# Kernel optimization log

Measured on AMD Instinct MI355X. Metric: run time of the kernel, lower is better.

## Reference

```python
import jax, jax.numpy as jnp
import numpy as np

N = 100000   # graph nodes
E = 600000   # edges
D = 128      # feature_dim
K = 3        # candidate ops per MixedOp
EPS = 1e-5   # BatchNorm eps


def _param_stack(key, n_ops):
    kW, kb = jax.random.split(key)
    W = jax.random.normal(kW, (n_ops, K, D, D), jnp.float32) * (1.0 / np.sqrt(D))
    b = jax.random.normal(kb, (n_ops, K, D), jnp.float32) * 0.01
    g = jnp.ones((n_ops, K, D), jnp.float32)
    be = jnp.zeros((n_ops, K, D), jnp.float32)
    return W, b, g, be


def setup_inputs() -> dict:
    key = jax.random.key(0)
    ks = jax.random.split(key, 16)
    inp = {
        'src_emb': jax.random.normal(ks[0], (N, D), jnp.float32),
        'hr': jax.random.normal(ks[1], (N, D), jnp.float32),
        'edge_src': jax.random.randint(ks[2], (E,), 0, N),
        'edge_dst': jax.random.randint(ks[3], (E,), 0, N),
        'weights_zero': jax.random.uniform(ks[4], (1, K), jnp.float32),
        'weights_first': jax.random.uniform(ks[5], (3, K), jnp.float32),
        'weights_middle': jax.random.uniform(ks[6], (2, K), jnp.float32),
        'weights_last': jax.random.uniform(ks[7], (2, K), jnp.float32),
    }
    for name, k, n_ops in [('zero', ks[8], 1), ('first', ks[9], 3), ('mid', ks[10], 2), ('last', ks[11], 2)]:
        W, b, g, be = _param_stack(k, n_ops)
        inp[f'W_{name}'] = W; inp[f'b_{name}'] = b
        inp[f'g_{name}'] = g; inp[f'be_{name}'] = be
    inp['W_cat'] = jax.random.normal(ks[12], (3 * D, D), jnp.float32) * (1.0 / np.sqrt(3 * D))
    inp['b_cat'] = jax.random.normal(ks[13], (D,), jnp.float32) * 0.01
    inp['g_cat'] = jnp.ones((D,), jnp.float32)
    inp['be_cat'] = jnp.zeros((D,), jnp.float32)
    return inp


def _mean_agg(h, src, dst):
    s = jax.ops.segment_sum(h[src], dst, num_segments=N)            # [N,D]
    deg = jax.ops.segment_sum(jnp.ones((src.shape[0],), h.dtype), dst, num_segments=N)
    return s / jnp.maximum(deg, 1.0)[:, None]


def _max_agg(h, src, dst):
    m = jax.ops.segment_max(h[src], dst, num_segments=N)            # -inf for empty segs
    return jnp.where(jnp.isfinite(m), m, 0.0)


def _mixed(cands, w, W, b, g, be):
    # cands: list of K [N,D]; w:[K]; W:[K,D,D]; b/g/be:[K,D]
    x = jnp.stack(cands)                                            # [K,N,D]
    y = jnp.einsum('knd,kdf->knf', x, W) + b[:, None, :]            # Linear per candidate
    mu = jnp.mean(y, axis=1, keepdims=True)                         # BatchNorm1d (batch stats)
    var = jnp.var(y, axis=1, keepdims=True)
    y = (y - mu) * jax.lax.rsqrt(var + EPS) * g[:, None, :] + be[:, None, :]
    y = jax.nn.relu(y)
    return jnp.einsum('k,knd->nd', w, y)                            # alpha-weighted sum


def _graph_cands(h, src, dst):
    return [h, _mean_agg(h, src, dst), _max_agg(h, src, dst)]


def _cell_forward(src_emb, hr, edge_src, edge_dst,
                  weights_zero, weights_first, weights_middle, weights_last,
                  W_zero, b_zero, g_zero, be_zero,
                  W_first, b_first, g_first, be_first,
                  W_mid, b_mid, g_mid, be_mid,
                  W_last, b_last, g_last, be_last,
                  W_cat, b_cat, g_cat, be_cat):
    src, dst = edge_src, edge_dst
    # Cell_Zero: relation-composition candidates on (src_emb, hr)
    pre = [src_emb, src_emb - hr, src_emb * hr]
    h_in = _mixed(pre, weights_zero[0], W_zero[0], b_zero[0], g_zero[0], be_zero[0])
    # Cell_First (nodes=2): ops layout [(i=0,j=0),(i=1,j=0),(i=1,j=1)]
    states = [h_in]
    s0 = _mixed(_graph_cands(states[0], src, dst), weights_first[0], W_first[0], b_first[0], g_first[0], be_first[0])
    states.append(s0)
    s1 = (_mixed(_graph_cands(states[0], src, dst), weights_first[1], W_first[1], b_first[1], g_first[1], be_first[1])
          + _mixed(_graph_cands(states[1], src, dst), weights_first[2], W_first[2], b_first[2], g_first[2], be_first[2]))
    states.append(s1)
    states = states[1:]                                             # drop h_in -> len 2
    # Cell_Middle (nodes=2): one MixedOp per state
    states = [_mixed(_graph_cands(states[i], src, dst), weights_middle[i], W_mid[i], b_mid[i], g_mid[i], be_mid[i])
              for i in range(2)]
    # Cell_Last (in_nodes=2, nodes=1): one new state from both inputs; returns all 3
    s_last = (_mixed(_graph_cands(states[0], src, dst), weights_last[0], W_last[0], b_last[0], g_last[0], be_last[0])
              + _mixed(_graph_cands(states[1], src, dst), weights_last[1], W_last[1], b_last[1], g_last[1], be_last[1]))
    states = states + [s_last]                                      # len 3
    # concat -> Linear -> BN -> ReLU (dropout p=0)
    h = jnp.concatenate(states, axis=1) @ W_cat + b_cat             # [N,D]
    mu = jnp.mean(h, axis=0, keepdims=True)
    var = jnp.var(h, axis=0, keepdims=True)
    h = (h - mu) * jax.lax.rsqrt(var + EPS) * g_cat + be_cat
    return jax.nn.relu(h)


def reference(src_emb, hr, edge_src, edge_dst,
              weights_zero, weights_first, weights_middle, weights_last,
              W_zero, b_zero, g_zero, be_zero,
              W_first, b_first, g_first, be_first,
              W_mid, b_mid, g_mid, be_mid,
              W_last, b_last, g_last, be_last,
              W_cat, b_cat, g_cat, be_cat):
    return _cell_forward(src_emb, hr, edge_src, edge_dst,
                         weights_zero, weights_first, weights_middle, weights_last,
                         W_zero, b_zero, g_zero, be_zero,
                         W_first, b_first, g_first, be_first,
                         W_mid, b_mid, g_mid, be_mid,
                         W_last, b_last, g_last, be_last,
                         W_cat, b_cat, g_cat, be_cat)
```

## Files before the change

### kernel.cpp

```cpp
#include <hip/hip_runtime.h>

#define N_NODES 100000
#define N_EDGES 600000
#define NPAD    100096
#define NTILES  782
#define SCAN_B  98
#define EPS_F   1e-5f

typedef __bf16 bf16_t;
typedef __bf16 bf16x8 __attribute__((ext_vector_type(8)));
typedef __bf16 bf16x4 __attribute__((ext_vector_type(4)));
typedef float  f32x4  __attribute__((ext_vector_type(4)));

__global__ __launch_bounds__(256)
void init_zero_kernel(int* __restrict__ deg, float* __restrict__ stats)
{
    int i = blockIdx.x * 256 + threadIdx.x;
    if (i < N_NODES) deg[i] = 0;
    if (i < 9 * 768) stats[i] = 0.f;
}

__global__ __launch_bounds__(256)
void transpose_w_kernel(const float* __restrict__ Wz, const float* __restrict__ Wf,
                        const float* __restrict__ Wm, const float* __restrict__ Wl,
                        const float* __restrict__ Wc, bf16_t* __restrict__ wt)
{
    int idx = blockIdx.x * 256 + threadIdx.x;
    int mat = idx >> 14;
    int off = idx & 16383;
    int n = off >> 7, kk = off & 127;
    const float* src;
    if      (mat < 3)  src = Wz + mat * 16384;
    else if (mat < 12) src = Wf + (mat - 3) * 16384;
    else if (mat < 18) src = Wm + (mat - 12) * 16384;
    else if (mat < 24) src = Wl + (mat - 18) * 16384;
    else               src = Wc + (mat - 24) * 16384;
    wt[idx] = (bf16_t)src[kk * 128 + n];
}

__global__ __launch_bounds__(256)
void pre_kernel(const float* __restrict__ se, const float* __restrict__ hr,
                bf16_t* __restrict__ p0, bf16_t* __restrict__ p1, bf16_t* __restrict__ p2)
{
    long i = ((long)blockIdx.x * 256 + threadIdx.x) * 8;
    float4 a0 = *(const float4*)&se[i], a1 = *(const float4*)&se[i + 4];
    float4 b0 = *(const float4*)&hr[i], b1 = *(const float4*)&hr[i + 4];
    float av[8] = {a0.x, a0.y, a0.z, a0.w, a1.x, a1.y, a1.z, a1.w};
    float bv[8] = {b0.x, b0.y, b0.z, b0.w, b1.x, b1.y, b1.z, b1.w};
    bf16x8 o0, o1, o2;
#pragma unroll
    for (int j = 0; j < 8; ++j) {
        o0[j] = (bf16_t)av[j];
        o1[j] = (bf16_t)(av[j] - bv[j]);
        o2[j] = (bf16_t)(av[j] * bv[j]);
    }
    *(bf16x8*)&p0[i] = o0;
    *(bf16x8*)&p1[i] = o1;
    *(bf16x8*)&p2[i] = o2;
}

__global__ __launch_bounds__(256)
void deg_count_kernel(const int* __restrict__ dst, int* __restrict__ deg)
{
    int i = blockIdx.x * 256 + threadIdx.x;
    if (i < N_EDGES) atomicAdd(&deg[dst[i]], 1);
}

__global__ __launch_bounds__(256)
void scan_a_kernel(const int* __restrict__ deg, int* __restrict__ partials)
{
    __shared__ int ls[256];
    int b = blockIdx.x, t = threadIdx.x;
    int s = 0;
    for (int j = 0; j < 4; ++j) {
        int i = b * 1024 + t * 4 + j;
        if (i < N_NODES) s += deg[i];
    }
    ls[t] = s; __syncthreads();
    for (int o = 128; o > 0; o >>= 1) {
        if (t < o) ls[t] += ls[t + o];
        __syncthreads();
    }
    if (t == 0) partials[b] = ls[0];
}

__global__ void scan_b_kernel(const int* __restrict__ partials, int* __restrict__ pofs)
{
    if (threadIdx.x == 0) {
        int a = 0;
        for (int i = 0; i < SCAN_B; ++i) { pofs[i] = a; a += partials[i]; }
    }
}

__global__ __launch_bounds__(256)
void scan_c_kernel(const int* __restrict__ deg, const int* __restrict__ pofs,
                   int* __restrict__ row_ptr, int* __restrict__ cursor)
{
    __shared__ int ls[256];
    int b = blockIdx.x, t = threadIdx.x;
    int v[4], s = 0;
    for (int j = 0; j < 4; ++j) {
        int i = b * 1024 + t * 4 + j;
        v[j] = (i < N_NODES) ? deg[i] : 0;
        s += v[j];
    }
    ls[t] = s; __syncthreads();
    for (int o = 1; o < 256; o <<= 1) {
        int tv = (t >= o) ? ls[t - o] : 0;
        __syncthreads();
        ls[t] += tv;
        __syncthreads();
    }
    int excl = ls[t] - s + pofs[b];
    for (int j = 0; j < 4; ++j) {
        int i = b * 1024 + t * 4 + j;
        if (i < N_NODES) { row_ptr[i] = excl; cursor[i] = excl; excl += v[j]; }
    }
    if (b == 0 && t == 0) row_ptr[N_NODES] = N_EDGES;
}

__global__ __launch_bounds__(256)
void scatter_kernel(const int* __restrict__ src, const int* __restrict__ dst,
                    int* __restrict__ cursor, int* __restrict__ csr_src)
{
    int i = blockIdx.x * 256 + threadIdx.x;
    if (i < N_EDGES) {
        int p = atomicAdd(&cursor[dst[i]], 1);
        csr_src[p] = src[i];
    }
}

__global__ __launch_bounds__(256)
void agg_kernel(const bf16_t* __restrict__ h, const int* __restrict__ row_ptr,
                const int* __restrict__ csr_src,
                bf16_t* __restrict__ mean_o, bf16_t* __restrict__ max_o)
{
    int node = blockIdx.x * 16 + (threadIdx.x >> 4);
    int dd = (threadIdx.x & 15) * 8;
    int e0 = row_ptr[node], e1 = row_ptr[node + 1];
    float s[8], mx[8];
#pragma unroll
    for (int j = 0; j < 8; ++j) { s[j] = 0.f; mx[j] = 0.f; }
    for (int e = e0; e < e1; ++e) {
        int sc = csr_src[e];
        bf16x8 v = *(const bf16x8*)&h[(long)sc * 128 + dd];
#pragma unroll
        for (int j = 0; j < 8; ++j) {
            float f = (float)v[j];
            s[j] += f;
            mx[j] = fmaxf(mx[j], f);
        }
    }
    float inv = 1.f / fmaxf((float)(e1 - e0), 1.f);
    bf16x8 om, ox;
#pragma unroll
    for (int j = 0; j < 8; ++j) { om[j] = (bf16_t)(s[j] * inv); ox[j] = (bf16_t)mx[j]; }
    *(bf16x8*)&mean_o[(long)node * 128 + dd] = om;
    *(bf16x8*)&max_o [(long)node * 128 + dd] = ox;
}

__global__ __launch_bounds__(256, 2)
void gemmA_kernel(const bf16_t* __restrict__ x0, const bf16_t* __restrict__ x1,
                  const bf16_t* __restrict__ x2, const bf16_t* __restrict__ wt,
                  float* __restrict__ partial, int mode)
{
    __shared__ bf16_t lds_w[16384];
    __shared__ bf16_t lds_x[16384];
    __shared__ float lred[512];
    const int tid  = threadIdx.x;
    const int lane = tid & 63;
    const int wave = tid >> 6;
    const int quad = lane >> 4;
    const int t16  = lane & 15;
    const int wr = wave >> 1, wc = wave & 1;
    const long tile_base = (long)blockIdx.x * 128;

    f32x4 acc[4][4];
#pragma unroll
    for (int a = 0; a < 4; ++a)
#pragma unroll
        for (int b = 0; b < 4; ++b) acc[a][b] = (f32x4){0.f, 0.f, 0.f, 0.f};

    const int k_sel = blockIdx.y;
    const int nchunk = (mode == 0) ? 1 : 3;
    const bf16_t* xk = (k_sel == 0) ? x0 : ((k_sel == 1) ? x1 : x2);

    for (int c3 = 0; c3 < nchunk; ++c3) {
        const bf16_t* xcur = (mode == 0) ? xk : ((c3 == 0) ? x0 : ((c3 == 1) ? x1 : x2));
        const bf16_t* wcur = (mode == 0) ? (wt + k_sel * 16384) : (wt + c3 * 16384);
        if (c3) __syncthreads();
#pragma unroll
        for (int i = 0; i < 8; ++i) {
            int idx = tid + i * 256;
            int row = idx >> 4, c = idx & 15;
            int sw = c ^ (row & 15);
            *(uint4*)&lds_w[row * 128 + sw * 8] = *(const uint4*)&wcur[row * 128 + c * 8];
            *(uint4*)&lds_x[row * 128 + sw * 8] = *(const uint4*)&xcur[(tile_base + row) * 128 + c * 8];
        }
        __syncthreads();
#pragma unroll
        for (int ks = 0; ks < 4; ++ks) {
            bf16x8 xf[4], wf[4];
#pragma unroll
            for (int ms = 0; ms < 4; ++ms) {
                int row = wr * 64 + ms * 16 + t16;
                int sw = (ks * 4 + quad) ^ t16;
                xf[ms] = *(const bf16x8*)&lds_x[row * 128 + sw * 8];
            }
#pragma unroll
            for (int ns = 0; ns < 4; ++ns) {
                int row = wc * 64 + ns * 16 + t16;
                int sw = (ks * 4 + quad) ^ t16;
                wf[ns] = *(const bf16x8*)&lds_w[row * 128 + sw * 8];
            }
#pragma unroll
            for (int ns = 0; ns < 4; ++ns)
#pragma unroll
                for (int ms = 0; ms < 4; ++ms)
                    acc[ns][ms] = __builtin_amdgcn_mfma_f32_16x16x32_bf16(
                        wf[ns], xf[ms], acc[ns][ms], 0, 0, 0);
        }
    }

    float ss[16], sq[16];
#pragma unroll
    for (int i = 0; i < 16; ++i) { ss[i] = 0.f; sq[i] = 0.f; }
#pragma unroll
    for (int ms = 0; ms < 4; ++ms) {
        long m = tile_base + wr * 64 + ms * 16 + t16;
        if (m < N_NODES) {
#pragma unroll
            for (int ns = 0; ns < 4; ++ns)
#pragma unroll
                for (int j = 0; j < 4; ++j) {
                    float v = acc[ns][ms][j];
                    ss[ns * 4 + j] += v;
                    sq[ns * 4 + j] += v * v;
                }
        }
    }
#pragma unroll
    for (int o = 1; o < 16; o <<= 1) {
#pragma unroll
        for (int i = 0; i < 16; ++i) {
            ss[i] += __shfl_xor(ss[i], o);
            sq[i] += __shfl_xor(sq[i], o);
        }
    }
    if (t16 == 0) {
#pragma unroll
        for (int i = 0; i < 16; ++i) {
            lred[wave * 128 + quad * 32 + i]      = ss[i];
            lred[wave * 128 + quad * 32 + 16 + i] = sq[i];
        }
    }
    asm volatile("s_waitcnt lgkmcnt(0)" ::: "memory");
    __builtin_amdgcn_s_barrier();
    {
        int t = tid;
        int d   = t & 127;
        int sel = (t >> 7) * 16;
        int dwc = d >> 6;
        int q   = (d >> 2) & 3;
        int i   = ((d >> 4) & 3) * 4 + (d & 3);
        float v = lred[(0 * 2 + dwc) * 128 + q * 32 + sel + i]
                + lred[(1 * 2 + dwc) * 128 + q * 32 + sel + i];
        long pidx = ((long)((mode == 0) ? k_sel : 0) * NTILES + blockIdx.x) * 256 + t;
        partial[pidx] = v;
    }
}

__global__ __launch_bounds__(256)
void reduce_stats_kernel(const float* __restrict__ partial, float* __restrict__ st)
{
    int k = blockIdx.x, j = blockIdx.y, t = threadIdx.x;
    int b0 = j * 98, b1 = (b0 + 98 < NTILES) ? b0 + 98 : NTILES;
    float s = 0.f;
    const float* p = partial + (long)k * NTILES * 256 + t;
    for (int b = b0; b < b1; ++b) s += p[(long)b * 256];
    atomicAdd(&st[k * 256 + t], s);
}

__global__ __launch_bounds__(256)
void coef_kernel(const float* __restrict__ st, const float* __restrict__ bias,
                 const float* __restrict__ gg, const float* __restrict__ be,
                 const float* __restrict__ wmix, float* __restrict__ coef, int mode)
{
    int t = threadIdx.x;
    if (t >= 128) return;
    const float invN = 1.0f / (float)N_NODES;
    int nk = (mode == 0) ? 3 : 1;
    for (int k = 0; k < nk; ++k) {
        float S = st[k * 256 + t], Q = st[k * 256 + 128 + t];
        float sa  = S * invN;
        float var = Q * invN - sa * sa;
        float rs  = rsqrtf(var + EPS_F);
        float gk = gg[k * 128 + t], bek = be[k * 128 + t];
        float wk = (mode == 0) ? wmix[k] : 1.f;
        coef[k * 256 + t]       = wk * rs * gk;
        coef[k * 256 + 128 + t] = wk * (-sa * rs * gk + bek);
        (void)bias;
    }
}

__global__ __launch_bounds__(256, 2)
void gemmB_kernel(const bf16_t* __restrict__ x0, const bf16_t* __restrict__ x1,
                  const bf16_t* __restrict__ x2, const bf16_t* __restrict__ wt,
                  const float* __restrict__ coef, bf16_t* __restrict__ outb,
                  float* __restrict__ outf, int mode, int accflag)
{
    __shared__ bf16_t lds_w[16384];
    __shared__ bf16_t lds_x[16384];
    __shared__ float lsc[768];
    const int tid  = threadIdx.x;
    const int lane = tid & 63;
    const int wave = tid >> 6;
    const int quad = lane >> 4;
    const int t16  = lane & 15;
    const int wr = wave >> 1, wc = wave & 1;
    const long tile_base = (long)blockIdx.x * 128;

    lsc[tid] = coef[tid];
    if (tid < 256) { lsc[tid + 256] = coef[tid + 256]; lsc[tid + 512] = coef[tid + 512]; }

    f32x4 acc[4][4], res[4][4];
#pragma unroll
    for (int a = 0; a < 4; ++a)
#pragma unroll
        for (int b = 0; b < 4; ++b) acc[a][b] = (f32x4){0.f, 0.f, 0.f, 0.f};

    if (mode == 0 && accflag) {
#pragma unroll
        for (int ns = 0; ns < 4; ++ns)
#pragma unroll
            for (int ms = 0; ms < 4; ++ms) {
                long m = tile_base + wr * 64 + ms * 16 + t16;
                int n0 = wc * 64 + ns * 16 + quad * 4;
                bf16x4 pv = *(const bf16x4*)&outb[(m < N_NODES ? m : 0) * 128 + n0];
                res[ns][ms] = (f32x4){(float)pv[0], (float)pv[1], (float)pv[2], (float)pv[3]};
            }
    } else {
#pragma unroll
        for (int a = 0; a < 4; ++a)
#pragma unroll
            for (int b = 0; b < 4; ++b) res[a][b] = (f32x4){0.f, 0.f, 0.f, 0.f};
    }

    for (int c3 = 0; c3 < 3; ++c3) {
        const bf16_t* xcur = (c3 == 0) ? x0 : ((c3 == 1) ? x1 : x2);
        const bf16_t* wcur = wt + c3 * 16384;
        __syncthreads();
#pragma unroll
        for (int i = 0; i < 8; ++i) {
            int idx = tid + i * 256;
            int row = idx >> 4, c = idx & 15;
            int sw = c ^ (row & 15);
            *(uint4*)&lds_w[row * 128 + sw * 8] = *(const uint4*)&wcur[row * 128 + c * 8];
            *(uint4*)&lds_x[row * 128 + sw * 8] = *(const uint4*)&xcur[(tile_base + row) * 128 + c * 8];
        }
        __syncthreads();
        if (mode == 0) {
#pragma unroll
            for (int a = 0; a < 4; ++a)
#pragma unroll
                for (int b = 0; b < 4; ++b) acc[a][b] = (f32x4){0.f, 0.f, 0.f, 0.f};
        }
#pragma unroll
        for (int ks = 0; ks < 4; ++ks) {
            bf16x8 xf[4], wf[4];
#pragma unroll
            for (int ms = 0; ms < 4; ++ms) {
                int row = wr * 64 + ms * 16 + t16;
                int sw = (ks * 4 + quad) ^ t16;
                xf[ms] = *(const bf16x8*)&lds_x[row * 128 + sw * 8];
            }
#pragma unroll
            for (int ns = 0; ns < 4; ++ns) {
                int row = wc * 64 + ns * 16 + t16;
                int sw = (ks * 4 + quad) ^ t16;
                wf[ns] = *(const bf16x8*)&lds_w[row * 128 + sw * 8];
            }
#pragma unroll
            for (int ns = 0; ns < 4; ++ns)
#pragma unroll
                for (int ms = 0; ms < 4; ++ms)
                    acc[ns][ms] = __builtin_amdgcn_mfma_f32_16x16x32_bf16(
                        wf[ns], xf[ms], acc[ns][ms], 0, 0, 0);
        }
        if (mode == 0) {
#pragma unroll
            for (int ns = 0; ns < 4; ++ns) {
                int n0 = wc * 64 + ns * 16 + quad * 4;
                float4 A4 = *(const float4*)&lsc[c3 * 256 + n0];
                float4 B4 = *(const float4*)&lsc[c3 * 256 + 128 + n0];
#pragma unroll
                for (int ms = 0; ms < 4; ++ms) {
                    res[ns][ms][0] += fmaxf(acc[ns][ms][0] * A4.x + B4.x, 0.f);
                    res[ns][ms][1] += fmaxf(acc[ns][ms][1] * A4.y + B4.y, 0.f);
                    res[ns][ms][2] += fmaxf(acc[ns][ms][2] * A4.z + B4.z, 0.f);
                    res[ns][ms][3] += fmaxf(acc[ns][ms][3] * A4.w + B4.w, 0.f);
                }
            }
        }
    }

    if (mode == 0) {
#pragma unroll
        for (int ms = 0; ms < 4; ++ms) {
            long m = tile_base + wr * 64 + ms * 16 + t16;
            if (m < N_NODES) {
#pragma unroll
                for (int ns = 0; ns < 4; ++ns) {
                    int n0 = wc * 64 + ns * 16 + quad * 4;
                    bf16x4 ov;
                    ov[0] = (bf16_t)res[ns][ms][0];
                    ov[1] = (bf16_t)res[ns][ms][1];
                    ov[2] = (bf16_t)res[ns][ms][2];
                    ov[3] = (bf16_t)res[ns][ms][3];
                    *(bf16x4*)&outb[m * 128 + n0] = ov;
                }
            }
        }
    } else {
#pragma unroll
        for (int ms = 0; ms < 4; ++ms) {
            long m = tile_base + wr * 64 + ms * 16 + t16;
            if (m < N_NODES) {
#pragma unroll
                for (int ns = 0; ns < 4; ++ns) {
                    int n0 = wc * 64 + ns * 16 + quad * 4;
                    float4 A4 = *(const float4*)&lsc[n0];
                    float4 B4 = *(const float4*)&lsc[128 + n0];
                    float4 o;
                    o.x = fmaxf(acc[ns][ms][0] * A4.x + B4.x, 0.f);
                    o.y = fmaxf(acc[ns][ms][1] * A4.y + B4.y, 0.f);
                    o.z = fmaxf(acc[ns][ms][2] * A4.z + B4.z, 0.f);
                    o.w = fmaxf(acc[ns][ms][3] * A4.w + B4.w, 0.f);
                    *(float4*)&outf[m * 128 + n0] = o;
                }
            }
        }
    }
}

extern "C" void kernel_launch(void* const* d_in, const int* in_sizes, int n_in,
                              void* d_out, int out_size, void* d_ws, size_t ws_size,
                              hipStream_t stream)
{
    const float* src_emb = (const float*)d_in[0];
    const float* hr      = (const float*)d_in[1];
    const int*   e_src   = (const int*)d_in[2];
    const int*   e_dst   = (const int*)d_in[3];
    const float* w_zero  = (const float*)d_in[4];
    const float* w_first = (const float*)d_in[5];
    const float* w_mid   = (const float*)d_in[6];
    const float* w_last  = (const float*)d_in[7];
    const float* W_zero  = (const float*)d_in[8];
    const float* b_zero  = (const float*)d_in[9];
    const float* g_zero  = (const float*)d_in[10];
    const float* be_zero = (const float*)d_in[11];
    const float* W_first = (const float*)d_in[12];
    const float* b_first = (const float*)d_in[13];
    const float* g_first = (const float*)d_in[14];
    const float* be_first= (const float*)d_in[15];
    const float* W_mid   = (const float*)d_in[16];
    const float* b_mid   = (const float*)d_in[17];
    const float* g_mid   = (const float*)d_in[18];
    const float* be_mid  = (const float*)d_in[19];
    const float* W_last  = (const float*)d_in[20];
    const float* b_last  = (const float*)d_in[21];
    const float* g_last  = (const float*)d_in[22];
    const float* be_last = (const float*)d_in[23];
    const float* W_cat   = (const float*)d_in[24];
    const float* b_cat   = (const float*)d_in[25];
    const float* g_cat   = (const float*)d_in[26];
    const float* be_cat  = (const float*)d_in[27];
    float* out = (float*)d_out;

    char* ws = (char*)d_ws;
    size_t off = 0;
    auto carve = [&](size_t bytes) -> char* {
        off = (off + 255) & ~(size_t)255;
        char* p = ws + off;
        off += bytes;
        return p;
    };

    const size_t SB = (size_t)NPAD * 128 * sizeof(bf16_t);
    bf16_t* B[8];
    for (int i = 0; i < 8; ++i) B[i] = (bf16_t*)carve(SB);
    bf16_t* wt    = (bf16_t*)carve((size_t)27 * 16384 * 2);
    float*  stats = (float*)carve(9 * 768 * sizeof(float));
    float*  partial = (float*)carve((size_t)3 * NTILES * 256 * sizeof(float));
    float*  coefs = (float*)carve(768 * sizeof(float));
    int* deg    = (int*)carve((size_t)N_NODES * 4);
    int* rowp   = (int*)carve((size_t)(N_NODES + 1) * 4);
    int* cursor = (int*)carve((size_t)N_NODES * 4);
    int* csr    = (int*)carve((size_t)N_EDGES * 4);
    int* parts  = (int*)carve(SCAN_B * 4);
    int* pofs   = (int*)carve(SCAN_B * 4);

    bf16_t* wtZ  = wt;
    bf16_t* wtF0 = wt + (size_t)3  * 16384;
    bf16_t* wtF1 = wt + (size_t)6  * 16384;
    bf16_t* wtF2 = wt + (size_t)9  * 16384;
    bf16_t* wtM0 = wt + (size_t)12 * 16384;
    bf16_t* wtM1 = wt + (size_t)15 * 16384;
    bf16_t* wtL0 = wt + (size_t)18 * 16384;
    bf16_t* wtL1 = wt + (size_t)21 * 16384;
    bf16_t* wtC  = wt + (size_t)24 * 16384;

    const int GEL8 = (N_NODES * 128) / 2048;

    init_zero_kernel<<<dim3((N_NODES + 255) / 256), dim3(256), 0, stream>>>(deg, stats);
    transpose_w_kernel<<<dim3(1728), dim3(256), 0, stream>>>(W_zero, W_first, W_mid, W_last, W_cat, wt);
    deg_count_kernel<<<dim3((N_EDGES + 255) / 256), dim3(256), 0, stream>>>(e_dst, deg);
    scan_a_kernel<<<dim3(SCAN_B), dim3(256), 0, stream>>>(deg, parts);
    scan_b_kernel<<<dim3(1), dim3(64), 0, stream>>>(parts, pofs);
    scan_c_kernel<<<dim3(SCAN_B), dim3(256), 0, stream>>>(deg, pofs, rowp, cursor);
    scatter_kernel<<<dim3((N_EDGES + 255) / 256), dim3(256), 0, stream>>>(e_src, e_dst, cursor, csr);

    auto M = [&](const bf16_t* x0_, const bf16_t* x1_, const bf16_t* x2_,
                 const bf16_t* w_, const float* b_, const float* g_, const float* be_,
                 const float* wm_, bf16_t* ob_, float* of_, float* st_,
                 int acc_, int mode_) {
        int nk = (mode_ == 0) ? 3 : 1;
        gemmA_kernel<<<dim3(NTILES, nk), dim3(256), 0, stream>>>(
            x0_, x1_, x2_, w_, partial, mode_);
        reduce_stats_kernel<<<dim3(nk, 8), dim3(256), 0, stream>>>(partial, st_);
        coef_kernel<<<dim3(1), dim3(256), 0, stream>>>(st_, b_, g_, be_, wm_, coefs, mode_);
        gemmB_kernel<<<dim3(NTILES), dim3(256), 0, stream>>>(
            x0_, x1_, x2_, w_, coefs, ob_, of_, mode_, acc_);
    };
    auto A = [&](const bf16_t* h_, bf16_t* me_, bf16_t* mx_) {
        agg_kernel<<<dim3(N_NODES / 16), dim3(256), 0, stream>>>(h_, rowp, csr, me_, mx_);
    };

    float* st0 = stats + 0 * 768;
    float* st1 = stats + 1 * 768;
    float* st2 = stats + 2 * 768;
    float* st3 = stats + 3 * 768;
    float* st4 = stats + 4 * 768;
    float* st5 = stats + 5 * 768;
    float* st6 = stats + 6 * 768;
    float* st7 = stats + 7 * 768;
    float* st8 = stats + 8 * 768;

    pre_kernel<<<dim3(GEL8), dim3(256), 0, stream>>>(src_emb, hr, B[3], B[4], B[5]);
    M(B[3], B[4], B[5], wtZ, b_zero, g_zero, be_zero, w_zero, B[6], nullptr, st0, 0, 0);

    A(B[6], B[3], B[4]);

    M(B[6], B[3], B[4], wtF0, b_first + 0, g_first + 0, be_first + 0,
      w_first + 0, B[5], nullptr, st1, 0, 0);
    M(B[6], B[3], B[4], wtF1, b_first + 384, g_first + 384, be_first + 384,
      w_first + 3, B[7], nullptr, st2, 0, 0);

    A(B[5], B[3], B[4]);

    M(B[5], B[3], B[4], wtF2, b_first + 768, g_first + 768, be_first + 768,
      w_first + 6, B[7], nullptr, st3, 1, 0);
    M(B[5], B[3], B[4], wtM0, b_mid + 0, g_mid + 0, be_mid + 0,
      w_mid + 0, B[6], nullptr, st4, 0, 0);

    A(B[7], B[3], B[4]);

    M(B[7], B[3], B[4], wtM1, b_mid + 384, g_mid + 384, be_mid + 384,
      w_mid + 3, B[5], nullptr, st5, 0, 0);

    A(B[6], B[3], B[4]);
    M(B[6], B[3], B[4], wtL0, b_last + 0, g_last + 0, be_last + 0,
      w_last + 0, B[7], nullptr, st6, 0, 0);
    A(B[5], B[3], B[4]);
    M(B[5], B[3], B[4], wtL1, b_last + 384, g_last + 384, be_last + 384,
      w_last + 3, B[7], nullptr, st7, 1, 0);

    M(B[6], B[5], B[7], wtC, b_cat, g_cat, be_cat, nullptr,
      nullptr, out, st8, 0, 1);
}
```

Before: 1.284 ms.

## Fuse paired MixedOps sharing inputs into dual GEMM kernels and inline coef

Adds gemmA2/gemmB2 kernels that compute two MixedOps sharing the same three input tensors in one pass, staging each X tile once and reusing it for both weight sets. This removes repeated input loads and launches. The coef kernel is also removed and the BN coefficients are computed inside gemmB from the stats, saving one launch per op. In exchange gemmB2 holds two result register arrays, which raises register pressure, and its launch bounds drop the 2-block occupancy hint.

```diff
diff --git a/kernel.cpp b/kernel.cpp
--- a/kernel.cpp
+++ b/kernel.cpp
@@ -11,6 +11,106 @@
 typedef __bf16 bf16x8 __attribute__((ext_vector_type(8)));
 typedef __bf16 bf16x4 __attribute__((ext_vector_type(4)));
 typedef float  f32x4  __attribute__((ext_vector_type(4)));
+
+#define STAGE_WX(WSRC, XSRC) do { \
+    _Pragma("unroll") for (int i_ = 0; i_ < 8; ++i_) { \
+        int idx_ = tid + i_ * 256; \
+        int row_ = idx_ >> 4, c_ = idx_ & 15; \
+        int sw_ = c_ ^ (row_ & 15); \
+        *(uint4*)&lds_w[row_ * 128 + sw_ * 8] = *(const uint4*)&(WSRC)[row_ * 128 + c_ * 8]; \
+        *(uint4*)&lds_x[row_ * 128 + sw_ * 8] = *(const uint4*)&(XSRC)[(tile_base + row_) * 128 + c_ * 8]; \
+    } } while (0)
+
+#define STAGE_W(WSRC) do { \
+    _Pragma("unroll") for (int i_ = 0; i_ < 8; ++i_) { \
+        int idx_ = tid + i_ * 256; \
+        int row_ = idx_ >> 4, c_ = idx_ & 15; \
+        int sw_ = c_ ^ (row_ & 15); \
+        *(uint4*)&lds_w[row_ * 128 + sw_ * 8] = *(const uint4*)&(WSRC)[row_ * 128 + c_ * 8]; \
+    } } while (0)
+
+#define ZACC() do { \
+    _Pragma("unroll") for (int a_ = 0; a_ < 4; ++a_) \
+    _Pragma("unroll") for (int b_ = 0; b_ < 4; ++b_) \
+        acc[a_][b_] = (f32x4){0.f, 0.f, 0.f, 0.f}; } while (0)
+
+#define MMAC() do { \
+    _Pragma("unroll") for (int ks = 0; ks < 4; ++ks) { \
+        bf16x8 xf[4], wf[4]; \
+        _Pragma("unroll") for (int ms = 0; ms < 4; ++ms) { \
+            int row_ = wr * 64 + ms * 16 + t16; \
+            int sw_ = (ks * 4 + quad) ^ t16; \
+            xf[ms] = *(const bf16x8*)&lds_x[row_ * 128 + sw_ * 8]; \
+        } \
+        _Pragma("unroll") for (int ns = 0; ns < 4; ++ns) { \
+            int row_ = wc * 64 + ns * 16 + t16; \
+            int sw_ = (ks * 4 + quad) ^ t16; \
+            wf[ns] = *(const bf16x8*)&lds_w[row_ * 128 + sw_ * 8]; \
+        } \
+        _Pragma("unroll") for (int ns = 0; ns < 4; ++ns) \
+        _Pragma("unroll") for (int ms = 0; ms < 4; ++ms) \
+            acc[ns][ms] = __builtin_amdgcn_mfma_f32_16x16x32_bf16( \
+                wf[ns], xf[ms], acc[ns][ms], 0, 0, 0); \
+    } } while (0)
+
+#define STATS(SLICE) do { \
+    float ss[16], sq[16]; \
+    _Pragma("unroll") for (int i_ = 0; i_ < 16; ++i_) { ss[i_] = 0.f; sq[i_] = 0.f; } \
+    _Pragma("unroll") for (int ms = 0; ms < 4; ++ms) { \
+        long m_ = tile_base + wr * 64 + ms * 16 + t16; \
+        if (m_ < N_NODES) { \
+            _Pragma("unroll") for (int ns = 0; ns < 4; ++ns) \
+            _Pragma("unroll") for (int j_ = 0; j_ < 4; ++j_) { \
+                float v_ = acc[ns][ms][j_]; \
+                ss[ns * 4 + j_] += v_; sq[ns * 4 + j_] += v_ * v_; \
+            } \
+        } \
+    } \
+    _Pragma("unroll") for (int o_ = 1; o_ < 16; o_ <<= 1) \
+    _Pragma("unroll") for (int i_ = 0; i_ < 16; ++i_) { \
+        ss[i_] += __shfl_xor(ss[i_], o_); sq[i_] += __shfl_xor(sq[i_], o_); \
+    } \
+    if (t16 == 0) { \
+        _Pragma("unroll") for (int i_ = 0; i_ < 16; ++i_) { \
+            lred[wave * 128 + quad * 32 + i_]      = ss[i_]; \
+            lred[wave * 128 + quad * 32 + 16 + i_] = sq[i_]; \
+        } \
+    } \
+    asm volatile("s_waitcnt lgkmcnt(0)" ::: "memory"); \
+    __builtin_amdgcn_s_barrier(); \
+    { \
+        int d_   = tid & 127; \
+        int sel_ = (tid >> 7) * 16; \
+        int dwc_ = d_ >> 6; \
+        int q_   = (d_ >> 2) & 3; \
+        int i_   = ((d_ >> 4) & 3) * 4 + (d_ & 3); \
+        float v_ = lred[(0 * 2 + dwc_) * 128 + q_ * 32 + sel_ + i_] \
+                 + lred[(1 * 2 + dwc_) * 128 + q_ * 32 + sel_ + i_]; \
+        partial[((long)(SLICE) * NTILES + blockIdx.x) * 256 + tid] = v_; \
+    } } while (0)
+
+#define FOLD(RES, LB) do { \
+    _Pragma("unroll") for (int ns = 0; ns < 4; ++ns) { \
+        int n0_ = wc * 64 + ns * 16 + quad * 4; \
+        float4 A4_ = *(const float4*)&lsc[(LB) + n0_]; \
+        float4 B4_ = *(const float4*)&lsc[(LB) + 128 + n0_]; \
+        _Pragma("unroll") for (int ms = 0; ms < 4; ++ms) { \
+            RES[ns][ms][0] += fmaxf(acc[ns][ms][0] * A4_.x + B4_.x, 0.f); \
+            RES[ns][ms][1] += fmaxf(acc[ns][ms][1] * A4_.y + B4_.y, 0.f); \
+            RES[ns][ms][2] += fmaxf(acc[ns][ms][2] * A4_.z + B4_.z, 0.f); \
+            RES[ns][ms][3] += fmaxf(acc[ns][ms][3] * A4_.w + B4_.w, 0.f); \
+        } \
+    } } while (0)
+
+#define COEF_TO_LSC(ST, GG, BE, WK, LB) do { \
+    float S_ = (ST)[k_ * 256 + tid], Q_ = (ST)[k_ * 256 + 128 + tid]; \
+    float sa_  = S_ * invN; \
+    float var_ = Q_ * invN - sa_ * sa_; \
+    float rs_  = rsqrtf(var_ + EPS_F); \
+    float gk_ = (GG)[k_ * 128 + tid], bek_ = (BE)[k_ * 128 + tid]; \
+    lsc[(LB) + k_ * 256 + tid]       = (WK) * rs_ * gk_; \
+    lsc[(LB) + k_ * 256 + 128 + tid] = (WK) * (-sa_ * rs_ * gk_ + bek_); \
+    } while (0)
 
 __global__ __launch_bounds__(256)
 void init_zero_kernel(int* __restrict__ deg, float* __restrict__ stats)
@@ -176,10 +276,7 @@
     const long tile_base = (long)blockIdx.x * 128;
 
     f32x4 acc[4][4];
-#pragma unroll
-    for (int a = 0; a < 4; ++a)
-#pragma unroll
-        for (int b = 0; b < 4; ++b) acc[a][b] = (f32x4){0.f, 0.f, 0.f, 0.f};
+    ZACC();
 
     const int k_sel = blockIdx.y;
     const int nchunk = (mode == 0) ? 1 : 3;
@@ -189,85 +286,45 @@
         const bf16_t* xcur = (mode == 0) ? xk : ((c3 == 0) ? x0 : ((c3 == 1) ? x1 : x2));
         const bf16_t* wcur = (mode == 0) ? (wt + k_sel * 16384) : (wt + c3 * 16384);
         if (c3) __syncthreads();
-#pragma unroll
-        for (int i = 0; i < 8; ++i) {
-            int idx = tid + i * 256;
-            int row = idx >> 4, c = idx & 15;
-            int sw = c ^ (row & 15);
-            *(uint4*)&lds_w[row * 128 + sw * 8] = *(const uint4*)&wcur[row * 128 + c * 8];
-            *(uint4*)&lds_x[row * 128 + sw * 8] = *(const uint4*)&xcur[(tile_base + row) * 128 + c * 8];
-        }
-        __syncthreads();
-#pragma unroll
-        for (int ks = 0; ks < 4; ++ks) {
-            bf16x8 xf[4], wf[4];
-#pragma unroll
-            for (int ms = 0; ms < 4; ++ms) {
-                int row = wr * 64 + ms * 16 + t16;
-                int sw = (ks * 4 + quad) ^ t16;
-                xf[ms] = *(const bf16x8*)&lds_x[row * 128 + sw * 8];
-            }
-#pragma unroll
-            for (int ns = 0; ns < 4; ++ns) {
-                int row = wc * 64 + ns * 16 + t16;
-                int sw = (ks * 4 + quad) ^ t16;
-                wf[ns] = *(const bf16x8*)&lds_w[row * 128 + sw * 8];
-            }
-#pragma unroll
-            for (int ns = 0; ns < 4; ++ns)
-#pragma unroll
-                for (int ms = 0; ms < 4; ++ms)
-                    acc[ns][ms] = __builtin_amdgcn_mfma_f32_16x16x32_bf16(
-                        wf[ns], xf[ms], acc[ns][ms], 0, 0, 0);
-        }
-    }
-
-    float ss[16], sq[16];
-#pragma unroll
-    for (int i = 0; i < 16; ++i) { ss[i] = 0.f; sq[i] = 0.f; }
-#pragma unroll
-    for (int ms = 0; ms < 4; ++ms) {
-        long m = tile_base + wr * 64 + ms * 16 + t16;
-        if (m < N_NODES) {
-#pragma unroll
-            for (int ns = 0; ns < 4; ++ns)
-#pragma unroll
-                for (int j = 0; j < 4; ++j) {
-                    float v = acc[ns][ms][j];
-                    ss[ns * 4 + j] += v;
-                    sq[ns * 4 + j] += v * v;
-                }
-        }
-    }
-#pragma unroll
-    for (int o = 1; o < 16; o <<= 1) {
-#pragma unroll
-        for (int i = 0; i < 16; ++i) {
-            ss[i] += __shfl_xor(ss[i], o);
-            sq[i] += __shfl_xor(sq[i], o);
-        }
-    }
-    if (t16 == 0) {
-#pragma unroll
-        for (int i = 0; i < 16; ++i) {
-            lred[wave * 128 + quad * 32 + i]      = ss[i];
-            lred[wave * 128 + quad * 32 + 16 + i] = sq[i];
-        }
-    }
-    asm volatile("s_waitcnt lgkmcnt(0)" ::: "memory");
-    __builtin_amdgcn_s_barrier();
-    {
-        int t = tid;
-        int d   = t & 127;
-        int sel = (t >> 7) * 16;
-        int dwc = d >> 6;
-        int q   = (d >> 2) & 3;
-        int i   = ((d >> 4) & 3) * 4 + (d & 3);
-        float v = lred[(0 * 2 + dwc) * 128 + q * 32 + sel + i]
-                + lred[(1 * 2 + dwc) * 128 + q * 32 + sel + i];
-        long pidx = ((long)((mode == 0) ? k_sel : 0) * NTILES + blockIdx.x) * 256 + t;
-        partial[pidx] = v;
-    }
+        STAGE_WX(wcur, xcur);
+        __syncthreads();
+        MMAC();
+    }
+    STATS((mode == 0) ? k_sel : 0);
+}
+
+__global__ __launch_bounds__(256, 2)
+void gemmA2_kernel(const bf16_t* __restrict__ x0, const bf16_t* __restrict__ x1,
+                   const bf16_t* __restrict__ x2, const bf16_t* __restrict__ wta,
+                   const bf16_t* __restrict__ wtb, float* __restrict__ partial)
+{
+    __shared__ bf16_t lds_w[16384];
+    __shared__ bf16_t lds_x[16384];
+    __shared__ float lred[512];
+    const int tid  = threadIdx.x;
+    const int lane = tid & 63;
+    const int wave = tid >> 6;
+    const int quad = lane >> 4;
+    const int t16  = lane & 15;
+    const int wr = wave >> 1, wc = wave & 1;
+    const long tile_base = (long)blockIdx.x * 128;
+
+    f32x4 acc[4][4];
+    const int k_sel = blockIdx.y;
+    const bf16_t* xk = (k_sel == 0) ? x0 : ((k_sel == 1) ? x1 : x2);
+
+    STAGE_WX(wta + k_sel * 16384, xk);
+    __syncthreads();
+    ZACC();
+    MMAC();
+    STATS(k_sel);
+
+    __syncthreads();
+    STAGE_W(wtb + k_sel * 16384);
+    __syncthreads();
+    ZACC();
+    MMAC();
+    STATS(3 + k_sel);
 }
 
 __global__ __launch_bounds__(256)
@@ -281,32 +338,12 @@
     atomicAdd(&st[k * 256 + t], s);
 }
 
-__global__ __launch_bounds__(256)
-void coef_kernel(const float* __restrict__ st, const float* __restrict__ bias,
-                 const float* __restrict__ gg, const float* __restrict__ be,
-                 const float* __restrict__ wmix, float* __restrict__ coef, int mode)
-{
-    int t = threadIdx.x;
-    if (t >= 128) return;
-    const float invN = 1.0f / (float)N_NODES;
-    int nk = (mode == 0) ? 3 : 1;
-    for (int k = 0; k < nk; ++k) {
-        float S = st[k * 256 + t], Q = st[k * 256 + 128 + t];
-        float sa  = S * invN;
-        float var = Q * invN - sa * sa;
-        float rs  = rsqrtf(var + EPS_F);
-        float gk = gg[k * 128 + t], bek = be[k * 128 + t];
-        float wk = (mode == 0) ? wmix[k] : 1.f;
-        coef[k * 256 + t]       = wk * rs * gk;
-        coef[k * 256 + 128 + t] = wk * (-sa * rs * gk + bek);
-        (void)bias;
-    }
-}
-
 __global__ __launch_bounds__(256, 2)
 void gemmB_kernel(const bf16_t* __restrict__ x0, const bf16_t* __restrict__ x1,
                   const bf16_t* __restrict__ x2, const bf16_t* __restrict__ wt,
-                  const float* __restrict__ coef, bf16_t* __restrict__ outb,
+                  const float* __restrict__ st, const float* __restrict__ bias,
+                  const float* __restrict__ gg, const float* __restrict__ be,
+                  const float* __restrict__ wmix, bf16_t* __restrict__ outb,
                   float* __restrict__ outf, int mode, int accflag)
 {
     __shared__ bf16_t lds_w[16384];
@@ -319,15 +356,19 @@
     const int t16  = lane & 15;
     const int wr = wave >> 1, wc = wave & 1;
     const long tile_base = (long)blockIdx.x * 128;
-
-    lsc[tid] = coef[tid];
-    if (tid < 256) { lsc[tid + 256] = coef[tid + 256]; lsc[tid + 512] = coef[tid + 512]; }
+    const float invN = 1.0f / (float)N_NODES;
+
+    if (tid < 128) {
+        int nk = (mode == 0) ? 3 : 1;
+        for (int k_ = 0; k_ < nk; ++k_) {
+            float wk = (mode == 0) ? wmix[k_] : 1.f;
+            COEF_TO_LSC(st, gg, be, wk, 0);
+        }
+    }
+    (void)bias;
 
     f32x4 acc[4][4], res[4][4];
-#pragma unroll
-    for (int a = 0; a < 4; ++a)
-#pragma unroll
-        for (int b = 0; b < 4; ++b) acc[a][b] = (f32x4){0.f, 0.f, 0.f, 0.f};
+    ZACC();
 
     if (mode == 0 && accflag) {
 #pragma unroll
@@ -350,58 +391,11 @@
         const bf16_t* xcur = (c3 == 0) ? x0 : ((c3 == 1) ? x1 : x2);
         const bf16_t* wcur = wt + c3 * 16384;
         __syncthreads();
-#pragma unroll
-        for (int i = 0; i < 8; ++i) {
-            int idx = tid + i * 256;
-            int row = idx >> 4, c = idx & 15;
-            int sw = c ^ (row & 15);
-            *(uint4*)&lds_w[row * 128 + sw * 8] = *(const uint4*)&wcur[row * 128 + c * 8];
-            *(uint4*)&lds_x[row * 128 + sw * 8] = *(const uint4*)&xcur[(tile_base + row) * 128 + c * 8];
-        }
-        __syncthreads();
-        if (mode == 0) {
-#pragma unroll
-            for (int a = 0; a < 4; ++a)
-#pragma unroll
-                for (int b = 0; b < 4; ++b) acc[a][b] = (f32x4){0.f, 0.f, 0.f, 0.f};
-        }
-#pragma unroll
-        for (int ks = 0; ks < 4; ++ks) {
-            bf16x8 xf[4], wf[4];
-#pragma unroll
-            for (int ms = 0; ms < 4; ++ms) {
-                int row = wr * 64 + ms * 16 + t16;
-                int sw = (ks * 4 + quad) ^ t16;
-                xf[ms] = *(const bf16x8*)&lds_x[row * 128 + sw * 8];
-            }
-#pragma unroll
-            for (int ns = 0; ns < 4; ++ns) {
-                int row = wc * 64 + ns * 16 + t16;
-                int sw = (ks * 4 + quad) ^ t16;
-                wf[ns] = *(const bf16x8*)&lds_w[row * 128 + sw * 8];
-            }
-#pragma unroll
-            for (int ns = 0; ns < 4; ++ns)
-#pragma unroll
-                for (int ms = 0; ms < 4; ++ms)
-                    acc[ns][ms] = __builtin_amdgcn_mfma_f32_16x16x32_bf16(
-                        wf[ns], xf[ms], acc[ns][ms], 0, 0, 0);
-        }
-        if (mode == 0) {
-#pragma unroll
-            for (int ns = 0; ns < 4; ++ns) {
-                int n0 = wc * 64 + ns * 16 + quad * 4;
-                float4 A4 = *(const float4*)&lsc[c3 * 256 + n0];
-                float4 B4 = *(const float4*)&lsc[c3 * 256 + 128 + n0];
-#pragma unroll
-                for (int ms = 0; ms < 4; ++ms) {
-                    res[ns][ms][0] += fmaxf(acc[ns][ms][0] * A4.x + B4.x, 0.f);
-                    res[ns][ms][1] += fmaxf(acc[ns][ms][1] * A4.y + B4.y, 0.f);
-                    res[ns][ms][2] += fmaxf(acc[ns][ms][2] * A4.z + B4.z, 0.f);
-                    res[ns][ms][3] += fmaxf(acc[ns][ms][3] * A4.w + B4.w, 0.f);
-                }
-            }
-        }
+        STAGE_WX(wcur, xcur);
+        __syncthreads();
+        if (mode == 0) ZACC();
+        MMAC();
+        if (mode == 0) FOLD(res, c3 * 256);
     }
 
     if (mode == 0) {
@@ -438,6 +432,92 @@
                     o.w = fmaxf(acc[ns][ms][3] * A4.w + B4.w, 0.f);
                     *(float4*)&outf[m * 128 + n0] = o;
                 }
+            }
+        }
+    }
+}
+
+__global__ __launch_bounds__(256)
+void gemmB2_kernel(const bf16_t* __restrict__ x0, const bf16_t* __restrict__ x1,
+                   const bf16_t* __restrict__ x2, const bf16_t* __restrict__ wta,
+                   const bf16_t* __restrict__ wtb,
+                   const float* __restrict__ sta, const float* __restrict__ stb,
+                   const float* __restrict__ gga, const float* __restrict__ bea,
+                   const float* __restrict__ wma,
+                   const float* __restrict__ ggb, const float* __restrict__ beb,
+                   const float* __restrict__ wmb,
+                   bf16_t* __restrict__ outa, bf16_t* __restrict__ outbb,
+                   int acca, int accb)
+{
+    __shared__ bf16_t lds_w[16384];
+    __shared__ bf16_t lds_x[16384];
+    __shared__ float lsc[1536];
+    const int tid  = threadIdx.x;
+    const int lane = tid & 63;
+    const int wave = tid >> 6;
+    const int quad = lane >> 4;
+    const int t16  = lane & 15;
+    const int wr = wave >> 1, wc = wave & 1;
+    const long tile_base = (long)blockIdx.x * 128;
+    const float invN = 1.0f / (float)N_NODES;
+
+    if (tid < 128) {
+        for (int k_ = 0; k_ < 3; ++k_) {
+            COEF_TO_LSC(sta, gga, bea, wma[k_], 0);
+            COEF_TO_LSC(stb, ggb, beb, wmb[k_], 768);
+        }
+    }
+
+    f32x4 acc[4][4], resa[4][4], resb[4][4];
+    ZACC();
+
+#pragma unroll
+    for (int ns = 0; ns < 4; ++ns)
+#pragma unroll
+        for (int ms = 0; ms < 4; ++ms) {
+            long m = tile_base + wr * 64 + ms * 16 + t16;
+            long mc = (m < N_NODES ? m : 0);
+            int n0 = wc * 64 + ns * 16 + quad * 4;
+            if (acca) {
+                bf16x4 pv = *(const bf16x4*)&outa[mc * 128 + n0];
+                resa[ns][ms] = (f32x4){(float)pv[0], (float)pv[1], (float)pv[2], (float)pv[3]};
+            } else resa[ns][ms] = (f32x4){0.f, 0.f, 0.f, 0.f};
+            if (accb) {
+                bf16x4 pv = *(const bf16x4*)&outbb[mc * 128 + n0];
+                resb[ns][ms] = (f32x4){(float)pv[0], (float)pv[1], (float)pv[2], (float)pv[3]};
+            } else resb[ns][ms] = (f32x4){0.f, 0.f, 0.f, 0.f};
+        }
+
+    for (int c3 = 0; c3 < 3; ++c3) {
+        const bf16_t* xcur = (c3 == 0) ? x0 : ((c3 == 1) ? x1 : x2);
+        __syncthreads();
+        STAGE_WX(wta + c3 * 16384, xcur);
+        __syncthreads();
+        ZACC();
+        MMAC();
+        FOLD(resa, c3 * 256);
+        __syncthreads();
+        STAGE_W(wtb + c3 * 16384);
+        __syncthreads();
+        ZACC();
+        MMAC();
+        FOLD(resb, 768 + c3 * 256);
+    }
+
+#pragma unroll
+    for (int ms = 0; ms < 4; ++ms) {
+        long m = tile_base + wr * 64 + ms * 16 + t16;
+        if (m < N_NODES) {
+#pragma unroll
+            for (int ns = 0; ns < 4; ++ns) {
+                int n0 = wc * 64 + ns * 16 + quad * 4;
+                bf16x4 ova, ovb;
+                ova[0] = (bf16_t)resa[ns][ms][0]; ova[1] = (bf16_t)resa[ns][ms][1];
+                ova[2] = (bf16_t)resa[ns][ms][2]; ova[3] = (bf16_t)resa[ns][ms][3];
+                ovb[0] = (bf16_t)resb[ns][ms][0]; ovb[1] = (bf16_t)resb[ns][ms][1];
+                ovb[2] = (bf16_t)resb[ns][ms][2]; ovb[3] = (bf16_t)resb[ns][ms][3];
+                *(bf16x4*)&outa [m * 128 + n0] = ova;
+                *(bf16x4*)&outbb[m * 128 + n0] = ovb;
             }
         }
     }
@@ -491,8 +571,7 @@
     for (int i = 0; i < 8; ++i) B[i] = (bf16_t*)carve(SB);
     bf16_t* wt    = (bf16_t*)carve((size_t)27 * 16384 * 2);
     float*  stats = (float*)carve(9 * 768 * sizeof(float));
-    float*  partial = (float*)carve((size_t)3 * NTILES * 256 * sizeof(float));
-    float*  coefs = (float*)carve(768 * sizeof(float));
+    float*  partial = (float*)carve((size_t)6 * NTILES * 256 * sizeof(float));
     int* deg    = (int*)carve((size_t)N_NODES * 4);
     int* rowp   = (int*)carve((size_t)(N_NODES + 1) * 4);
     int* cursor = (int*)carve((size_t)N_NODES * 4);
@@ -510,32 +589,6 @@
     bf16_t* wtL1 = wt + (size_t)21 * 16384;
     bf16_t* wtC  = wt + (size_t)24 * 16384;
 
-    const int GEL8 = (N_NODES * 128) / 2048;
-
-    init_zero_kernel<<<dim3((N_NODES + 255) / 256), dim3(256), 0, stream>>>(deg, stats);
-    transpose_w_kernel<<<dim3(1728), dim3(256), 0, stream>>>(W_zero, W_first, W_mid, W_last, W_cat, wt);
-    deg_count_kernel<<<dim3((N_EDGES + 255) / 256), dim3(256), 0, stream>>>(e_dst, deg);
-    scan_a_kernel<<<dim3(SCAN_B), dim3(256), 0, stream>>>(deg, parts);
-    scan_b_kernel<<<dim3(1), dim3(64), 0, stream>>>(parts, pofs);
-    scan_c_kernel<<<dim3(SCAN_B), dim3(256), 0, stream>>>(deg, pofs, rowp, cursor);
-    scatter_kernel<<<dim3((N_EDGES + 255) / 256), dim3(256), 0, stream>>>(e_src, e_dst, cursor, csr);
-
-    auto M = [&](const bf16_t* x0_, const bf16_t* x1_, const bf16_t* x2_,
-                 const bf16_t* w_, const float* b_, const float* g_, const float* be_,
-                 const float* wm_, bf16_t* ob_, float* of_, float* st_,
-                 int acc_, int mode_) {
-        int nk = (mode_ == 0) ? 3 : 1;
-        gemmA_kernel<<<dim3(NTILES, nk), dim3(256), 0, stream>>>(
-            x0_, x1_, x2_, w_, partial, mode_);
-        reduce_stats_kernel<<<dim3(nk, 8), dim3(256), 0, stream>>>(partial, st_);
-        coef_kernel<<<dim3(1), dim3(256), 0, stream>>>(st_, b_, g_, be_, wm_, coefs, mode_);
-        gemmB_kernel<<<dim3(NTILES), dim3(256), 0, stream>>>(
-            x0_, x1_, x2_, w_, coefs, ob_, of_, mode_, acc_);
-    };
-    auto A = [&](const bf16_t* h_, bf16_t* me_, bf16_t* mx_) {
-        agg_kernel<<<dim3(N_NODES / 16), dim3(256), 0, stream>>>(h_, rowp, csr, me_, mx_);
-    };
-
     float* st0 = stats + 0 * 768;
     float* st1 = stats + 1 * 768;
     float* st2 = stats + 2 * 768;
@@ -546,22 +599,59 @@
     float* st7 = stats + 7 * 768;
     float* st8 = stats + 8 * 768;
 
+    const int GEL8 = (N_NODES * 128) / 2048;
+
+    init_zero_kernel<<<dim3((N_NODES + 255) / 256), dim3(256), 0, stream>>>(deg, stats);
+    transpose_w_kernel<<<dim3(1728), dim3(256), 0, stream>>>(W_zero, W_first, W_mid, W_last, W_cat, wt);
+    deg_count_kernel<<<dim3((N_EDGES + 255) / 256), dim3(256), 0, stream>>>(e_dst, deg);
+    scan_a_kernel<<<dim3(SCAN_B), dim3(256), 0, stream>>>(deg, parts);
+    scan_b_kernel<<<dim3(1), dim3(64), 0, stream>>>(parts, pofs);
+    scan_c_kernel<<<dim3(SCAN_B), dim3(256), 0, stream>>>(deg, pofs, rowp, cursor);
+    scatter_kernel<<<dim3((N_EDGES + 255) / 256), dim3(256), 0, stream>>>(e_src, e_dst, cursor, csr);
+
+    auto A = [&](const bf16_t* h_, bf16_t* me_, bf16_t* mx_) {
+        agg_kernel<<<dim3(N_NODES / 16), dim3(256), 0, stream>>>(h_, rowp, csr, me_, mx_);
+    };
+    auto M = [&](const bf16_t* x0_, const bf16_t* x1_, const bf16_t* x2_,
+                 const bf16_t* w_, const float* b_, const float* g_, const float* be_,
+                 const float* wm_, bf16_t* ob_, float* of_, float* st_,
+                 int acc_, int mode_) {
+        int nk = (mode_ == 0) ? 3 : 1;
+        gemmA_kernel<<<dim3(NTILES, nk), dim3(256), 0, stream>>>(
+            x0_, x1_, x2_, w_, partial, mode_);
+        reduce_stats_kernel<<<dim3(nk, 8), dim3(256), 0, stream>>>(partial, st_);
+        gemmB_kernel<<<dim3(NTILES), dim3(256), 0, stream>>>(
+            x0_, x1_, x2_, w_, st_, b_, g_, be_, wm_, ob_, of_, mode_, acc_);
+    };
+    auto M2 = [&](const bf16_t* x0_, const bf16_t* x1_, const bf16_t* x2_,
+                  const bf16_t* wa_, const bf16_t* wb_, float* sta_, float* stb_,
+                  const float* ga_, const float* bea_, const float* wma_,
+                  const float* gb_, const float* beb_, const float* wmb_,
+                  bf16_t* oa_, bf16_t* ob_, int acca_, int accb_) {
+        gemmA2_kernel<<<dim3(NTILES, 3), dim3(256), 0, stream>>>(
+            x0_, x1_, x2_, wa_, wb_, partial);
+        reduce_stats_kernel<<<dim3(6, 8), dim3(256), 0, stream>>>(partial, sta_);
+        gemmB2_kernel<<<dim3(NTILES), dim3(256), 0, stream>>>(
+            x0_, x1_, x2_, wa_, wb_, sta_, stb_,
+            ga_, bea_, wma_, gb_, beb_, wmb_, oa_, ob_, acca_, accb_);
+    };
+
     pre_kernel<<<dim3(GEL8), dim3(256), 0, stream>>>(src_emb, hr, B[3], B[4], B[5]);
     M(B[3], B[4], B[5], wtZ, b_zero, g_zero, be_zero, w_zero, B[6], nullptr, st0, 0, 0);
 
     A(B[6], B[3], B[4]);
 
-    M(B[6], B[3], B[4], wtF0, b_first + 0, g_first + 0, be_first + 0,
-      w_first + 0, B[5], nullptr, st1, 0, 0);
-    M(B[6], B[3], B[4], wtF1, b_first + 384, g_first + 384, be_first + 384,
-      w_first + 3, B[7], nullptr, st2, 0, 0);
+    M2(B[6], B[3], B[4], wtF0, wtF1, st1, st2,
+       g_first + 0,   be_first + 0,   w_first + 0,
+       g_first + 384, be_first + 384, w_first + 3,
+       B[5], B[7], 0, 0);
 
     A(B[5], B[3], B[4]);
 
-    M(B[5], B[3], B[4], wtF2, b_first + 768, g_first + 768, be_first + 768,
-      w_first + 6, B[7], nullptr, st3, 1, 0);
-    M(B[5], B[3], B[4], wtM0, b_mid + 0, g_mid + 0, be_mid + 0,
-      w_mid + 0, B[6], nullptr, st4, 0, 0);
+    M2(B[5], B[3], B[4], wtF2, wtM0, st3, st4,
+       g_first + 768, be_first + 768, w_first + 6,
+       g_mid + 0,     be_mid + 0,     w_mid + 0,
+       B[7], B[6], 1, 0);
 
     A(B[7], B[3], B[4]);
 
```

Measured after the change: 1.282 ms. No clear change (-0.2%).
